# Kernel tuning notes

Hardware: AMD Instinct MI355X
Metric: run time of the kernel (lower is better)

The kernel has to match this reference:

```python
import jax, jax.numpy as jnp
import numpy as np

PATCH = 14          # ViT patch size
NUM_CLUSTERS = 64   # num_queries (cluster_strategy='fixed')
NUM_ITERS = 30      # fixed iteration budget emulating the tol-based while loop
TOL = 1e-4          # convergence tolerance on (sum of center shifts)**2
EPS = 1e-10


def _normalize(x, axis=-1, eps=EPS):
    n = jnp.linalg.norm(x, axis=axis, keepdims=True)
    return x / jnp.maximum(n, eps)


def _kmeans(X, num_clusters, key):
    """Cosine-distance k-means. X: [N, C]. Returns (assignments [N], centers [K, C])."""
    N = X.shape[0]
    idx = jax.random.choice(key, N, shape=(num_clusters,), replace=False)
    centers0 = X[idx]                       # random-point initialization
    Xn = _normalize(X)                      # normalized once, reused every iter
    ones = jnp.ones((N,), X.dtype)

    def body(carry, _):
        centers, done = carry
        # pairwise cosine distance: 1 - cos_sim  -> [N, K]
        dis = 1.0 - Xn @ _normalize(centers).T
        assign = jnp.argmin(dis, axis=1)
        # per-cluster scatter-mean (vectorized replacement of the python loop)
        sums = jax.ops.segment_sum(X, assign, num_segments=num_clusters)
        counts = jax.ops.segment_sum(ones, assign, num_segments=num_clusters)
        new_centers = jnp.where(counts[:, None] > 0,
                                sums / jnp.maximum(counts, 1.0)[:, None],
                                centers)
        shift = jnp.sum(jnp.sqrt(jnp.sum((new_centers - centers) ** 2, axis=1)))
        new_done = done | (shift ** 2 < TOL)
        centers = jnp.where(done, centers, new_centers)  # freeze after convergence
        return (centers, new_done), None

    (centers, _), _ = jax.lax.scan(body, (centers0, jnp.array(False)), None, length=NUM_ITERS)
    assign = jnp.argmin(1.0 - Xn @ _normalize(centers).T, axis=1)
    return assign, centers


def setup_inputs() -> dict:
    key = jax.random.key(0)
    features = jax.random.normal(key, (1, 1024, 96, 96), dtype=jnp.float32)
    return {"features": features}


def reference(features):
    B, C, HP, WP = features.shape  # [1, 1024, 96, 96]
    X = features.transpose(0, 2, 3, 1).reshape(-1, C)  # [N, C], N = HP*WP
    _, centers = _kmeans(X, NUM_CLUSTERS, jax.random.key(42))
    # cluster_logits = cosine similarity between every token and every center
    logits = _normalize(X) @ _normalize(centers).T            # [N, K]
    logits = logits.reshape(B, HP, WP, NUM_CLUSTERS).transpose(0, 3, 1, 2)  # [1, K, HP, WP]
    H, W = HP * PATCH, WP * PATCH
    logits_up = jax.image.resize(logits, (B, NUM_CLUSTERS, H, W), method='bilinear')
    cluster_ids = jnp.argmax(logits_up, axis=1)               # [1, H, W]
    return cluster_ids, logits_up
```

## Files before the change

kernel.cpp:

```cpp
#include <hip/hip_runtime.h>
#include <stdint.h>

#define NN 9216
#define CCH 1024
#define KK 64
#define HP 96
#define SCALE 14
#define HH 1344
#define NUM_ITERS 30
#define TOLV 1e-4

typedef __attribute__((ext_vector_type(4))) double d4;

__device__ __forceinline__ void tf2x32(unsigned k0, unsigned k1, unsigned& x0, unsigned& x1) {
  unsigned ks2 = k0 ^ k1 ^ 0x1BD11BDAu;
  x0 += k0; x1 += k1;
#define TFR(r) { x0 += x1; x1 = (x1 << r) | (x1 >> (32 - r)); x1 ^= x0; }
  TFR(13) TFR(15) TFR(26) TFR(6)
  x0 += k1; x1 += ks2 + 1u;
  TFR(17) TFR(29) TFR(16) TFR(24)
  x0 += ks2; x1 += k0 + 2u;
  TFR(13) TFR(15) TFR(26) TFR(6)
  x0 += k0; x1 += k1 + 3u;
  TFR(17) TFR(29) TFR(16) TFR(24)
  x0 += k1; x1 += ks2 + 4u;
  TFR(13) TFR(15) TFR(26) TFR(6)
  x0 += ks2; x1 += k0 + 5u;
#undef TFR
}

__global__ __launch_bounds__(256) void k_rng(unsigned* bits1, unsigned* bits2, double* ssq) {
  int t = blockIdx.x * 256 + threadIdx.x;
  unsigned k1a = 0, k1b = 0; tf2x32(0u, 42u, k1a, k1b);
  unsigned s1a = 0, s1b = 1; tf2x32(0u, 42u, s1a, s1b);
  unsigned s2a = 0, s2b = 1; tf2x32(k1a, k1b, s2a, s2b);
  unsigned o0 = 0, o1 = (unsigned)t;
  tf2x32(s1a, s1b, o0, o1);
  bits1[t] = o0 ^ o1;
  o0 = 0; o1 = (unsigned)t;
  tf2x32(s2a, s2b, o0, o1);
  bits2[t] = o0 ^ o1;
  ssq[t] = 0.0;
}

__global__ __launch_bounds__(256) void k_rank(const unsigned* __restrict__ bits,
                                              const unsigned* __restrict__ vals,
                                              unsigned* __restrict__ out_perm) {
  __shared__ __align__(16) unsigned lb[NN];
  int tid = threadIdx.x;
  for (int idx = tid; idx < NN; idx += 256) lb[idx] = bits[idx];
  __syncthreads();
  int i = blockIdx.x * 256 + tid;
  unsigned kb = lb[i];
  const uint4* l4 = reinterpret_cast<const uint4*>(lb);
  int rank = 0;
  for (int jj = 0; jj < NN / 4; ++jj) {
    uint4 v = l4[jj];
    int j = jj * 4;
    rank += (v.x < kb) || (v.x == kb && (j + 0) < i);
    rank += (v.y < kb) || (v.y == kb && (j + 1) < i);
    rank += (v.z < kb) || (v.z == kb && (j + 2) < i);
    rank += (v.w < kb) || (v.w == kb && (j + 3) < i);
  }
  out_perm[rank] = vals ? vals[i] : (unsigned)i;
}

__global__ __launch_bounds__(256) void k_gather(const float* __restrict__ F,
                                                const unsigned* __restrict__ perm2,
                                                float* __restrict__ centers) {
  int k = blockIdx.x;
  unsigned n = perm2[k];
  for (int c = threadIdx.x; c < CCH; c += 256)
    centers[k * CCH + c] = F[(size_t)c * NN + n];
}

__global__ __launch_bounds__(256) void k_ssq(const float* __restrict__ F, double* __restrict__ ssq) {
  int n = blockIdx.x * 256 + threadIdx.x;
  int c0 = blockIdx.y * 64;
  double acc = 0.0;
#pragma unroll 4
  for (int ci = 0; ci < 64; ++ci) {
    double v = (double)F[(size_t)(c0 + ci) * NN + n];
    acc = fma(v, v, acc);
  }
  atomicAdd(&ssq[n], acc);
}

__global__ __launch_bounds__(256) void k_norm32(const double* __restrict__ ssq, float* __restrict__ n32) {
  int n = blockIdx.x * 256 + threadIdx.x;
  n32[n] = (float)sqrt(ssq[n]);
}

__global__ __launch_bounds__(256) void k_prep0(const float* __restrict__ centers,
                                               float* __restrict__ cnT,
                                               int* __restrict__ counts,
                                               double* __restrict__ shift,
                                               int* __restrict__ done) {
  __shared__ double red[256];
  int k = blockIdx.x, tid = threadIdx.x;
  double local = 0.0;
  for (int c = tid; c < CCH; c += 256) {
    double v = (double)centers[k * CCH + c];
    local = fma(v, v, local);
  }
  red[tid] = local; __syncthreads();
  for (int s = 128; s > 0; s >>= 1) { if (tid < s) red[tid] += red[tid + s]; __syncthreads(); }
  float nc = fmaxf((float)sqrt(red[0]), 1e-10f);
  for (int c = tid; c < CCH; c += 256)
    cnT[(size_t)c * KK + k] = centers[k * CCH + c] / nc;
  if (tid == 0) {
    counts[k] = 0;
    if (k == 0) { *done = 0; shift[0] = 0.0; shift[1] = 0.0; }
  }
}

__global__ void k_probe(int* __restrict__ rowT, int* __restrict__ colT, int* __restrict__ okm) {
  int l = threadIdx.x;
  d4 z = {0.0, 0.0, 0.0, 0.0};
  d4 v1 = __builtin_amdgcn_mfma_f64_16x16x4f64(ldexp(1.0, l), 1.0, z, 0, 0, 0);
  d4 v2 = __builtin_amdgcn_mfma_f64_16x16x4f64(1.0, ldexp(1.0, l), z, 0, 0, 0);
  d4 v3 = __builtin_amdgcn_mfma_f64_16x16x4f64(ldexp(1.0, l >> 4), ldexp(1.0, 10 * (l >> 4)), z, 0, 0, 0);
  const double CM = 281479271743489.0;
  const double P3 = 8594130945.0;
  bool good = true, ish1 = true;
#pragma unroll
  for (int r = 0; r < 4; ++r) {
    int i = -1, j = -1;
    for (int t = 0; t < 16; ++t) {
      if (v1[r] == ldexp(CM, t)) i = t;
      if (v2[r] == ldexp(CM, t)) j = t;
    }
    good = good && (i >= 0) && (j >= 0) && (v3[r] == P3);
    ish1 = ish1 && (i == 4 * (l >> 4) + r) && (j == (l & 15));
    rowT[4 * l + r] = i; colT[4 * l + r] = j;
  }
  unsigned long long mg = __ballot(good);
  unsigned long long mh = __ballot(ish1);
  if (l == 0) *okm = (mg == ~0ull && mh != ~0ull) ? 1 : 0;
}

template <int MODE>
__global__ __launch_bounds__(256) void k_assign_m(const float* __restrict__ F,
                                                  const float* __restrict__ n32,
                                                  const float* __restrict__ cnT,
                                                  int* __restrict__ assign,
                                                  int* __restrict__ counts,
                                                  float* __restrict__ logitsS,
                                                  double* __restrict__ shift,
                                                  const int* __restrict__ done,
                                                  const int* __restrict__ rowT,
                                                  const int* __restrict__ colT,
                                                  const int* __restrict__ okm,
                                                  int iter) {
  if (*okm == 0) return;
  constexpr int CK = 64, NT = CCH / CK;
  constexpr int ASTR = 40, BSTR = 72;
  __shared__ __align__(16) float As[2][CK][ASTR];
  __shared__ __align__(16) float Bs[2][CK][BSTR];
  const int tid = threadIdx.x;
  if (MODE == 0) {
    if (blockIdx.x == 0 && tid == 0) shift[iter & 1] = 0.0;
    if (*done) return;
  }
  const int n0 = blockIdx.x * 32;
  const int s_ci = tid >> 2, s_q = tid & 3;
  const int lane = tid & 63, w = tid >> 6;
  const int h = w & 1, q = w >> 1;
  const int arow  = h * 16 + (lane & 15);
  const int kq    = lane >> 4;
  const int bcol0 = q * 32 + (lane & 15);
  float dn[8];
#pragma unroll
  for (int j = 0; j < 4; ++j) {
    dn[j]     = fmaxf(n32[n0 + 4 * s_q + j], 1e-10f);
    dn[4 + j] = fmaxf(n32[n0 + 16 + 4 * s_q + j], 1e-10f);
  }
  d4 acc0 = {0.0, 0.0, 0.0, 0.0}, acc1 = {0.0, 0.0, 0.0, 0.0};
  {
    float4 a0 = *(const float4*)(F + (size_t)s_ci * NN + n0 + 4 * s_q);
    float4 a1 = *(const float4*)(F + (size_t)s_ci * NN + n0 + 16 + 4 * s_q);
    float4 b[4];
#pragma unroll
    for (int j = 0; j < 4; ++j)
      b[j] = *(const float4*)(cnT + (size_t)s_ci * KK + 16 * s_q + 4 * j);
    float4 w0, w1;
    w0.x = a0.x / dn[0]; w0.y = a0.y / dn[1]; w0.z = a0.z / dn[2]; w0.w = a0.w / dn[3];
    w1.x = a1.x / dn[4]; w1.y = a1.y / dn[5]; w1.z = a1.z / dn[6]; w1.w = a1.w / dn[7];
    *(float4*)&As[0][s_ci][4 * s_q]      = w0;
    *(float4*)&As[0][s_ci][16 + 4 * s_q] = w1;
#pragma unroll
    for (int j = 0; j < 4; ++j)
      *(float4*)&Bs[0][s_ci][16 * s_q + 4 * j] = b[j];
  }
  __syncthreads();

  for (int t = 0; t < NT; ++t) {
    const int buf = t & 1;
    float4 a0, a1, b[4];
    if (t + 1 < NT) {
      const int cb = CK * (t + 1);
      a0 = *(const float4*)(F + (size_t)(cb + s_ci) * NN + n0 + 4 * s_q);
      a1 = *(const float4*)(F + (size_t)(cb + s_ci) * NN + n0 + 16 + 4 * s_q);
#pragma unroll
      for (int j = 0; j < 4; ++j)
        b[j] = *(const float4*)(cnT + (size_t)(cb + s_ci) * KK + 16 * s_q + 4 * j);
    }
#pragma unroll
    for (int s = 0; s < CK / 4; ++s) {
      const int ci = 4 * s + kq;
      double av = (double)As[buf][ci][arow];
      double b0 = (double)Bs[buf][ci][bcol0];
      double b1 = (double)Bs[buf][ci][bcol0 + 16];
      acc0 = __builtin_amdgcn_mfma_f64_16x16x4f64(av, b0, acc0, 0, 0, 0);
      acc1 = __builtin_amdgcn_mfma_f64_16x16x4f64(av, b1, acc1, 0, 0, 0);
    }
    if (t + 1 < NT) {
      const int nb = buf ^ 1;
      float4 w0, w1;
      w0.x = a0.x / dn[0]; w0.y = a0.y / dn[1]; w0.z = a0.z / dn[2]; w0.w = a0.w / dn[3];
      w1.x = a1.x / dn[4]; w1.y = a1.y / dn[5]; w1.z = a1.z / dn[6]; w1.w = a1.w / dn[7];
      *(float4*)&As[nb][s_ci][4 * s_q]      = w0;
      *(float4*)&As[nb][s_ci][16 + 4 * s_q] = w1;
#pragma unroll
      for (int j = 0; j < 4; ++j)
        *(float4*)&Bs[nb][s_ci][16 * s_q + 4 * j] = b[j];
    }
    __syncthreads();
  }

  float* Sl = &As[0][0][0];
#pragma unroll
  for (int r = 0; r < 4; ++r) {
    int iD = rowT[4 * lane + r];
    int jD = colT[4 * lane + r];
    Sl[(h * 16 + iD) * KK + q * 32 + jD]      = (float)acc0[r];
    Sl[(h * 16 + iD) * KK + q * 32 + 16 + jD] = (float)acc1[r];
  }
  __syncthreads();
  if (MODE == 0) {
    if (tid < 32) {
      const float* row = &Sl[tid * KK];
      float best = 1.0f - row[0]; int bk = 0;
      for (int k = 1; k < KK; ++k) { float d = 1.0f - row[k]; if (d < best) { best = d; bk = k; } }
      assign[n0 + tid] = bk;
      atomicAdd(&counts[bk], 1);
    }
  } else {
    for (int idx = tid; idx < 32 * KK; idx += 256) {
      int k = idx >> 5, nj = idx & 31;
      logitsS[(size_t)k * NN + n0 + nj] = Sl[nj * KK + k];
    }
  }
}

template <int MODE>
__global__ __launch_bounds__(256) void k_assign_v(const float* __restrict__ F,
                                                  const float* __restrict__ n32,
                                                  const float* __restrict__ cnT,
                                                  int* __restrict__ assign,
                                                  int* __restrict__ counts,
                                                  float* __restrict__ logitsS,
                                                  double* __restrict__ shift,
                                                  const int* __restrict__ done,
                                                  const int* __restrict__ okm,
                                                  int iter) {
  if (*okm != 0) return;
  constexpr int TN = 32, CK = 32, NT = CCH / CK;
  __shared__ __align__(16) float As[2][CK][TN];
  __shared__ __align__(16) float Bs[2][CK][KK];
  const int tid = threadIdx.x;
  if (MODE == 0) {
    if (blockIdx.x == 0 && tid == 0) shift[iter & 1] = 0.0;
    if (*done) return;
  }
  const int n0 = blockIdx.x * TN;
  const int a_ci = tid >> 3, a_nq = tid & 7;
  const int b_ci = tid >> 4, b_kq = tid & 15;
  const int nq = tid & 7, kp = tid >> 3;
  const float* np4 = n32 + n0 + 4 * a_nq;
  float d0 = fmaxf(np4[0], 1e-10f), d1 = fmaxf(np4[1], 1e-10f);
  float d2 = fmaxf(np4[2], 1e-10f), d3 = fmaxf(np4[3], 1e-10f);
  double acc[4][2] = {{0, 0}, {0, 0}, {0, 0}, {0, 0}};
  {
    const float* g0 = cnT + (size_t)(b_ci) * KK + 4 * b_kq;
    const float* g1 = cnT + (size_t)(16 + b_ci) * KK + 4 * b_kq;
    float* l0 = &Bs[0][0][0] + tid * 4;
    float* l1 = &Bs[0][0][0] + 1024 + tid * 4;
    __builtin_amdgcn_global_load_lds((const __attribute__((address_space(1))) void*)g0,
                                     (__attribute__((address_space(3))) void*)l0, 16, 0, 0);
    __builtin_amdgcn_global_load_lds((const __attribute__((address_space(1))) void*)g1,
                                     (__attribute__((address_space(3))) void*)l1, 16, 0, 0);
    float4 va = *(const float4*)(F + (size_t)a_ci * NN + n0 + 4 * a_nq);
    float4 w;
    w.x = va.x / d0; w.y = va.y / d1; w.z = va.z / d2; w.w = va.w / d3;
    *(float4*)(&As[0][0][0] + tid * 4) = w;
  }
  __syncthreads();

  for (int t = 0; t < NT; ++t) {
    const int buf = t & 1, nbuf = buf ^ 1;
    float4 va;
    if (t + 1 < NT) {
      const int cc = CK * (t + 1);
      const float* g0 = cnT + (size_t)(cc + b_ci) * KK + 4 * b_kq;
      const float* g1 = cnT + (size_t)(cc + 16 + b_ci) * KK + 4 * b_kq;
      float* l0 = &Bs[nbuf][0][0] + tid * 4;
      float* l1 = &Bs[nbuf][0][0] + 1024 + tid * 4;
      __builtin_amdgcn_global_load_lds((const __attribute__((address_space(1))) void*)g0,
                                       (__attribute__((address_space(3))) void*)l0, 16, 0, 0);
      __builtin_amdgcn_global_load_lds((const __attribute__((address_space(1))) void*)g1,
                                       (__attribute__((address_space(3))) void*)l1, 16, 0, 0);
      va = *(const float4*)(F + (size_t)(cc + a_ci) * NN + n0 + 4 * a_nq);
    }
#pragma unroll 8
    for (int ci = 0; ci < CK; ++ci) {
      double b0 = (double)Bs[buf][ci][2 * kp + 0], b1 = (double)Bs[buf][ci][2 * kp + 1];
      double a0 = (double)As[buf][ci][4 * nq + 0], a1 = (double)As[buf][ci][4 * nq + 1];
      double a2 = (double)As[buf][ci][4 * nq + 2], a3 = (double)As[buf][ci][4 * nq + 3];
      acc[0][0] = fma(a0, b0, acc[0][0]); acc[0][1] = fma(a0, b1, acc[0][1]);
      acc[1][0] = fma(a1, b0, acc[1][0]); acc[1][1] = fma(a1, b1, acc[1][1]);
      acc[2][0] = fma(a2, b0, acc[2][0]); acc[2][1] = fma(a2, b1, acc[2][1]);
      acc[3][0] = fma(a3, b0, acc[3][0]); acc[3][1] = fma(a3, b1, acc[3][1]);
    }
    if (t + 1 < NT) {
      float4 w;
      w.x = va.x / d0; w.y = va.y / d1; w.z = va.z / d2; w.w = va.w / d3;
      *(float4*)(&As[nbuf][0][0] + tid * 4) = w;
    }
    __syncthreads();
  }

  float* Sl = &Bs[0][0][0];
#pragma unroll
  for (int r = 0; r < 4; ++r) {
    Sl[(4 * nq + r) * KK + 2 * kp + 0] = (float)acc[r][0];
    Sl[(4 * nq + r) * KK + 2 * kp + 1] = (float)acc[r][1];
  }
  __syncthreads();
  if (MODE == 0) {
    if (tid < TN) {
      const float* row = &Sl[tid * KK];
      float best = 1.0f - row[0]; int bk = 0;
      for (int k = 1; k < KK; ++k) { float d = 1.0f - row[k]; if (d < best) { best = d; bk = k; } }
      assign[n0 + tid] = bk;
      atomicAdd(&counts[bk], 1);
    }
  } else {
    for (int idx = tid; idx < TN * KK; idx += 256) {
      int k = idx >> 5, nj = idx & 31;
      logitsS[(size_t)k * NN + n0 + nj] = Sl[nj * KK + k];
    }
  }
}

__global__ __launch_bounds__(256) void k_segsum(const float* __restrict__ F,
                                                const int* __restrict__ assign,
                                                double* __restrict__ sums,
                                                const int* __restrict__ done) {
  if (*done) return;
  constexpr int NCOPY = 8, KP = KK + 2;
  __shared__ double bins[NCOPY][KP];
  int c = blockIdx.x, tid = threadIdx.x;
  int cp = tid & (NCOPY - 1);
  for (int idx = tid; idx < NCOPY * KP; idx += 256) (&bins[0][0])[idx] = 0.0;
  __syncthreads();
  for (int n = tid; n < NN; n += 256) {
    int a = assign[n];
    double v = (double)F[(size_t)c * NN + n];
    atomicAdd(&bins[cp][a], v);
  }
  __syncthreads();
  if (tid < KK) {
    double s = 0.0;
#pragma unroll
    for (int r = 0; r < NCOPY; ++r) s += bins[r][tid];
    sums[(size_t)tid * CCH + c] = s;
  }
}

__global__ __launch_bounds__(256) void k_update(float* __restrict__ centers,
                                                const double* __restrict__ sums,
                                                int* __restrict__ counts,
                                                double* __restrict__ shift,
                                                int* __restrict__ done,
                                                float* __restrict__ cnT,
                                                int iter) {
  __shared__ double red[256];
  int k = blockIdx.x, tid = threadIdx.x;
  bool mydone = false;
  if (iter > 0) {
    double s = shift[(iter - 1) & 1];
    mydone = (*done != 0) || (s * s < TOLV);
  }
  if (mydone) { if (tid == 0) *done = 1; return; }
  int cnt = counts[k];
  double local = 0.0, l2 = 0.0;
  float nc[4];
#pragma unroll
  for (int i = 0; i < 4; ++i) {
    int c = tid + 256 * i;
    float old = centers[k * CCH + c];
    float v = (cnt > 0) ? (float)(sums[k * CCH + c] / (double)cnt) : old;
    nc[i] = v;
    double d = (double)v - (double)old;
    local = fma(d, d, local);
    double dv = (double)v;
    l2 = fma(dv, dv, l2);
    centers[k * CCH + c] = v;
  }
  red[tid] = local; __syncthreads();
  for (int s = 128; s > 0; s >>= 1) { if (tid < s) red[tid] += red[tid + s]; __syncthreads(); }
  if (tid == 0) atomicAdd(&shift[iter & 1], sqrt(red[0]));
  __syncthreads();
  red[tid] = l2; __syncthreads();
  for (int s = 128; s > 0; s >>= 1) { if (tid < s) red[tid] += red[tid + s]; __syncthreads(); }
  float nrm = fmaxf((float)sqrt(red[0]), 1e-10f);
#pragma unroll
  for (int i = 0; i < 4; ++i) {
    int c = tid + 256 * i;
    cnT[(size_t)c * KK + k] = nc[i] / nrm;
  }
  if (tid == 0) counts[k] = 0;
}

__global__ __launch_bounds__(256) void k_upsample(const float* __restrict__ logitsS,
                                                  float* __restrict__ out) {
  __shared__ float P[2][KK][HP];
  const int oy = blockIdx.x;
  const int tid = threadIdx.x;
  const float inv = 1.0f / 14.0f;
  float s_y = ((float)oy + 0.5f) * inv - 0.5f;
  float fy = floorf(s_y);
  float wy1 = s_y - fy, wy0 = 1.0f - wy1;
  int y0 = (int)fy, y1 = y0 + 1;
  if (y0 < 0)      { y0 = 0;      y1 = 0;      wy0 = 1.0f; wy1 = 0.0f; }
  if (y1 > HP - 1) { y0 = HP - 1; y1 = HP - 1; wy0 = 1.0f; wy1 = 0.0f; }
  for (int idx = tid; idx < 2 * KK * HP; idx += 256) {
    int r = idx / (KK * HP);
    int rem = idx - r * (KK * HP);
    int k = rem / HP, x = rem - k * HP;
    P[r][k][x] = logitsS[(size_t)k * NN + (r ? y1 : y0) * HP + x];
  }
  __syncthreads();
  float* outL = out + (size_t)HH * HH;
  const size_t rowoff = (size_t)oy * HH;
  for (int j = 0; j < 6; ++j) {
    int ox = tid + 256 * j;
    if (ox >= HH) break;
    float s_x = ((float)ox + 0.5f) * inv - 0.5f;
    float fx = floorf(s_x);
    float wx1 = s_x - fx, wx0 = 1.0f - wx1;
    int x0 = (int)fx, x1 = x0 + 1;
    if (x0 < 0)      { x0 = 0;      x1 = 0;      wx0 = 1.0f; wx1 = 0.0f; }
    if (x1 > HP - 1) { x0 = HP - 1; x1 = HP - 1; wx0 = 1.0f; wx1 = 0.0f; }
    float best = 0.0f; int bk = 0;
    for (int k = 0; k < KK; ++k) {
      float t0 = fmaf(wy1, P[1][k][x0], wy0 * P[0][k][x0]);
      float t1 = fmaf(wy1, P[1][k][x1], wy0 * P[0][k][x1]);
      float v  = fmaf(wx1, t1, wx0 * t0);
      outL[(size_t)k * (HH * HH) + rowoff + ox] = v;
      if (k == 0 || v > best) { best = v; bk = k; }
    }
    out[rowoff + ox] = (float)bk;
  }
}

extern "C" void kernel_launch(void* const* d_in, const int* in_sizes, int n_in,
                              void* d_out, int out_size, void* d_ws, size_t ws_size,
                              hipStream_t stream) {
  const float* F = (const float*)d_in[0];
  float* out = (float*)d_out;
  char* ws = (char*)d_ws;
  double*   ssq     = (double*)(ws + 0);
  double*   shift2  = (double*)(ws + 0);
  float*    n32     = (float*)(ws + 73728);
  float*    centers = (float*)(ws + 110592);
  float*    cnT     = (float*)(ws + 372736);
  double*   sums    = (double*)(ws + 634880);
  float*    logitsS = (float*)(ws + 1159168);
  unsigned* bits1   = (unsigned*)(ws + 3518472);
  unsigned* bits2   = (unsigned*)(ws + 3555336);
  unsigned* perm1   = (unsigned*)(ws + 3592200);
  int*      rowT    = (int*)(ws + 3592208);
  int*      colT    = (int*)(ws + 3593232);
  int*      okm     = (int*)(ws + 3594256);
  unsigned* perm2   = (unsigned*)(ws + 3629064);
  int*      assign  = (int*)(ws + 3665928);
  int*      counts  = (int*)(ws + 3702792);
  int*      done    = (int*)(ws + 3703048);

  k_rng<<<36, 256, 0, stream>>>(bits1, bits2, ssq);
  k_rank<<<36, 256, 0, stream>>>(bits1, nullptr, perm1);
  k_rank<<<36, 256, 0, stream>>>(bits2, perm1, perm2);
  k_probe<<<1, 64, 0, stream>>>(rowT, colT, okm);
  k_gather<<<64, 256, 0, stream>>>(F, perm2, centers);
  k_ssq<<<dim3(36, 16), 256, 0, stream>>>(F, ssq);
  k_norm32<<<36, 256, 0, stream>>>(ssq, n32);
  k_prep0<<<64, 256, 0, stream>>>(centers, cnT, counts, shift2, done);

  for (int it = 0; it < NUM_ITERS; ++it) {
    k_assign_m<0><<<288, 256, 0, stream>>>(F, n32, cnT, assign, counts, logitsS, shift2, done, rowT, colT, okm, it);
    k_assign_v<0><<<288, 256, 0, stream>>>(F, n32, cnT, assign, counts, logitsS, shift2, done, okm, it);
    k_segsum<<<1024, 256, 0, stream>>>(F, assign, sums, done);
    k_update<<<64, 256, 0, stream>>>(centers, sums, counts, shift2, done, cnT, it);
  }
  k_assign_m<1><<<288, 256, 0, stream>>>(F, n32, cnT, assign, counts, logitsS, shift2, done, rowT, colT, okm, 0);
  k_assign_v<1><<<288, 256, 0, stream>>>(F, n32, cnT, assign, counts, logitsS, shift2, done, okm, 0);
  k_upsample<<<1344, 256, 0, stream>>>(logitsS, out);
}
```

Measured before the change: 2.663 ms.

## Retile MFMA assign kernel to 48-token blocks and drop fallback and prep kernels

The MFMA assignment kernel now covers 48 tokens per block with each wave owning 16 centers, so each B value read from shared memory feeds three MFMAs. The grid shrinks from 288 to 192 blocks. The scalar fallback kernel is removed, the probe no longer requires a non-identity layout, the RNG is folded into the rank kernels, and the gather is merged into the center prep. Sum-of-squares now uses per-slice partial sums instead of atomics. This cuts launches and shared-memory traffic, but with fewer blocks the device may be less fully occupied, and there is no longer a fallback when the MFMA probe fails.

```diff
diff --git a/kernel.cpp b/kernel.cpp
--- a/kernel.cpp
+++ b/kernel.cpp
@@ -29,26 +29,22 @@
 #undef TFR
 }
 
-__global__ __launch_bounds__(256) void k_rng(unsigned* bits1, unsigned* bits2, double* ssq) {
-  int t = blockIdx.x * 256 + threadIdx.x;
-  unsigned k1a = 0, k1b = 0; tf2x32(0u, 42u, k1a, k1b);
-  unsigned s1a = 0, s1b = 1; tf2x32(0u, 42u, s1a, s1b);
-  unsigned s2a = 0, s2b = 1; tf2x32(k1a, k1b, s2a, s2b);
-  unsigned o0 = 0, o1 = (unsigned)t;
-  tf2x32(s1a, s1b, o0, o1);
-  bits1[t] = o0 ^ o1;
-  o0 = 0; o1 = (unsigned)t;
-  tf2x32(s2a, s2b, o0, o1);
-  bits2[t] = o0 ^ o1;
-  ssq[t] = 0.0;
-}
-
-__global__ __launch_bounds__(256) void k_rank(const unsigned* __restrict__ bits,
-                                              const unsigned* __restrict__ vals,
+template <int WHICH>
+__global__ __launch_bounds__(256) void k_rank(const unsigned* __restrict__ vals,
                                               unsigned* __restrict__ out_perm) {
   __shared__ __align__(16) unsigned lb[NN];
   int tid = threadIdx.x;
-  for (int idx = tid; idx < NN; idx += 256) lb[idx] = bits[idx];
+  unsigned sa, sb;
+  if (WHICH == 1) { sa = 0; sb = 1; tf2x32(0u, 42u, sa, sb); }
+  else {
+    unsigned k1a = 0, k1b = 0; tf2x32(0u, 42u, k1a, k1b);
+    sa = 0; sb = 1; tf2x32(k1a, k1b, sa, sb);
+  }
+  for (int idx = tid; idx < NN; idx += 256) {
+    unsigned o0 = 0, o1 = (unsigned)idx;
+    tf2x32(sa, sb, o0, o1);
+    lb[idx] = o0 ^ o1;
+  }
   __syncthreads();
   int i = blockIdx.x * 256 + tid;
   unsigned kb = lb[i];
@@ -65,16 +61,7 @@
   out_perm[rank] = vals ? vals[i] : (unsigned)i;
 }
 
-__global__ __launch_bounds__(256) void k_gather(const float* __restrict__ F,
-                                                const unsigned* __restrict__ perm2,
-                                                float* __restrict__ centers) {
-  int k = blockIdx.x;
-  unsigned n = perm2[k];
-  for (int c = threadIdx.x; c < CCH; c += 256)
-    centers[k * CCH + c] = F[(size_t)c * NN + n];
-}
-
-__global__ __launch_bounds__(256) void k_ssq(const float* __restrict__ F, double* __restrict__ ssq) {
+__global__ __launch_bounds__(256) void k_ssq(const float* __restrict__ F, double* __restrict__ ssq_p) {
   int n = blockIdx.x * 256 + threadIdx.x;
   int c0 = blockIdx.y * 64;
   double acc = 0.0;
@@ -83,31 +70,46 @@
     double v = (double)F[(size_t)(c0 + ci) * NN + n];
     acc = fma(v, v, acc);
   }
-  atomicAdd(&ssq[n], acc);
-}
-
-__global__ __launch_bounds__(256) void k_norm32(const double* __restrict__ ssq, float* __restrict__ n32) {
+  ssq_p[(size_t)blockIdx.y * NN + n] = acc;
+}
+
+__global__ __launch_bounds__(256) void k_norm16(const double* __restrict__ ssq_p, float* __restrict__ n32) {
   int n = blockIdx.x * 256 + threadIdx.x;
-  n32[n] = (float)sqrt(ssq[n]);
-}
-
-__global__ __launch_bounds__(256) void k_prep0(const float* __restrict__ centers,
+  double acc = 0.0;
+#pragma unroll
+  for (int r = 0; r < 16; ++r) acc += ssq_p[(size_t)r * NN + n];
+  n32[n] = (float)sqrt(acc);
+}
+
+__global__ __launch_bounds__(256) void k_prep0(const float* __restrict__ F,
+                                               const unsigned* __restrict__ perm2,
+                                               float* __restrict__ centers,
                                                float* __restrict__ cnT,
                                                int* __restrict__ counts,
                                                double* __restrict__ shift,
                                                int* __restrict__ done) {
   __shared__ double red[256];
   int k = blockIdx.x, tid = threadIdx.x;
+  unsigned n = perm2[k];
   double local = 0.0;
-  for (int c = tid; c < CCH; c += 256) {
-    double v = (double)centers[k * CCH + c];
-    local = fma(v, v, local);
+  float cv[4];
+#pragma unroll
+  for (int i = 0; i < 4; ++i) {
+    int c = tid + 256 * i;
+    float v = F[(size_t)c * NN + n];
+    cv[i] = v;
+    centers[k * CCH + c] = v;
+    double dv = (double)v;
+    local = fma(dv, dv, local);
   }
   red[tid] = local; __syncthreads();
   for (int s = 128; s > 0; s >>= 1) { if (tid < s) red[tid] += red[tid + s]; __syncthreads(); }
   float nc = fmaxf((float)sqrt(red[0]), 1e-10f);
-  for (int c = tid; c < CCH; c += 256)
-    cnT[(size_t)c * KK + k] = centers[k * CCH + c] / nc;
+#pragma unroll
+  for (int i = 0; i < 4; ++i) {
+    int c = tid + 256 * i;
+    cnT[(size_t)c * KK + k] = cv[i] / nc;
+  }
   if (tid == 0) {
     counts[k] = 0;
     if (k == 0) { *done = 0; shift[0] = 0.0; shift[1] = 0.0; }
@@ -122,7 +124,7 @@
   d4 v3 = __builtin_amdgcn_mfma_f64_16x16x4f64(ldexp(1.0, l >> 4), ldexp(1.0, 10 * (l >> 4)), z, 0, 0, 0);
   const double CM = 281479271743489.0;
   const double P3 = 8594130945.0;
-  bool good = true, ish1 = true;
+  bool good = true;
 #pragma unroll
   for (int r = 0; r < 4; ++r) {
     int i = -1, j = -1;
@@ -131,63 +133,63 @@
       if (v2[r] == ldexp(CM, t)) j = t;
     }
     good = good && (i >= 0) && (j >= 0) && (v3[r] == P3);
-    ish1 = ish1 && (i == 4 * (l >> 4) + r) && (j == (l & 15));
     rowT[4 * l + r] = i; colT[4 * l + r] = j;
   }
   unsigned long long mg = __ballot(good);
-  unsigned long long mh = __ballot(ish1);
-  if (l == 0) *okm = (mg == ~0ull && mh != ~0ull) ? 1 : 0;
+  if (l == 0) *okm = (mg == ~0ull) ? 1 : 0;
 }
 
 template <int MODE>
-__global__ __launch_bounds__(256) void k_assign_m(const float* __restrict__ F,
-                                                  const float* __restrict__ n32,
-                                                  const float* __restrict__ cnT,
-                                                  int* __restrict__ assign,
-                                                  int* __restrict__ counts,
-                                                  float* __restrict__ logitsS,
-                                                  double* __restrict__ shift,
-                                                  const int* __restrict__ done,
-                                                  const int* __restrict__ rowT,
-                                                  const int* __restrict__ colT,
-                                                  const int* __restrict__ okm,
-                                                  int iter) {
-  if (*okm == 0) return;
-  constexpr int CK = 64, NT = CCH / CK;
-  constexpr int ASTR = 40, BSTR = 72;
+__global__ __launch_bounds__(256) void k_assign(const float* __restrict__ F,
+                                                const float* __restrict__ n32,
+                                                const float* __restrict__ cnT,
+                                                int* __restrict__ assign,
+                                                int* __restrict__ counts,
+                                                float* __restrict__ logitsS,
+                                                double* __restrict__ shift,
+                                                const int* __restrict__ done,
+                                                const int* __restrict__ rowT,
+                                                const int* __restrict__ colT,
+                                                const int* __restrict__ okm,
+                                                int iter) {
+  constexpr int TN = 48, CK = 64, NT = CCH / CK;
+  constexpr int ASTR = 56, BSTR = 72;
   __shared__ __align__(16) float As[2][CK][ASTR];
   __shared__ __align__(16) float Bs[2][CK][BSTR];
   const int tid = threadIdx.x;
+  if (*okm == 0) return;
   if (MODE == 0) {
     if (blockIdx.x == 0 && tid == 0) shift[iter & 1] = 0.0;
     if (*done) return;
   }
-  const int n0 = blockIdx.x * 32;
+  const int n0 = blockIdx.x * TN;
   const int s_ci = tid >> 2, s_q = tid & 3;
   const int lane = tid & 63, w = tid >> 6;
-  const int h = w & 1, q = w >> 1;
-  const int arow  = h * 16 + (lane & 15);
-  const int kq    = lane >> 4;
-  const int bcol0 = q * 32 + (lane & 15);
-  float dn[8];
-#pragma unroll
-  for (int j = 0; j < 4; ++j) {
-    dn[j]     = fmaxf(n32[n0 + 4 * s_q + j], 1e-10f);
-    dn[4 + j] = fmaxf(n32[n0 + 16 + 4 * s_q + j], 1e-10f);
-  }
-  d4 acc0 = {0.0, 0.0, 0.0, 0.0}, acc1 = {0.0, 0.0, 0.0, 0.0};
+  const int col = lane & 15, kq = lane >> 4;
+  const int bcol = 16 * w + col;
+  float dn[12];
+#pragma unroll
+  for (int m = 0; m < 3; ++m)
+#pragma unroll
+    for (int j = 0; j < 4; ++j)
+      dn[4 * m + j] = fmaxf(n32[n0 + 16 * m + 4 * s_q + j], 1e-10f);
+  d4 acc[3] = {{0,0,0,0},{0,0,0,0},{0,0,0,0}};
+
   {
-    float4 a0 = *(const float4*)(F + (size_t)s_ci * NN + n0 + 4 * s_q);
-    float4 a1 = *(const float4*)(F + (size_t)s_ci * NN + n0 + 16 + 4 * s_q);
-    float4 b[4];
+    float4 a[3], b[4];
+#pragma unroll
+    for (int m = 0; m < 3; ++m)
+      a[m] = *(const float4*)(F + (size_t)s_ci * NN + n0 + 16 * m + 4 * s_q);
 #pragma unroll
     for (int j = 0; j < 4; ++j)
       b[j] = *(const float4*)(cnT + (size_t)s_ci * KK + 16 * s_q + 4 * j);
-    float4 w0, w1;
-    w0.x = a0.x / dn[0]; w0.y = a0.y / dn[1]; w0.z = a0.z / dn[2]; w0.w = a0.w / dn[3];
-    w1.x = a1.x / dn[4]; w1.y = a1.y / dn[5]; w1.z = a1.z / dn[6]; w1.w = a1.w / dn[7];
-    *(float4*)&As[0][s_ci][4 * s_q]      = w0;
-    *(float4*)&As[0][s_ci][16 + 4 * s_q] = w1;
+#pragma unroll
+    for (int m = 0; m < 3; ++m) {
+      float4 ww;
+      ww.x = a[m].x / dn[4*m+0]; ww.y = a[m].y / dn[4*m+1];
+      ww.z = a[m].z / dn[4*m+2]; ww.w = a[m].w / dn[4*m+3];
+      *(float4*)&As[0][s_ci][16 * m + 4 * s_q] = ww;
+    }
 #pragma unroll
     for (int j = 0; j < 4; ++j)
       *(float4*)&Bs[0][s_ci][16 * s_q + 4 * j] = b[j];
@@ -196,11 +198,12 @@
 
   for (int t = 0; t < NT; ++t) {
     const int buf = t & 1;
-    float4 a0, a1, b[4];
+    float4 a[3], b[4];
     if (t + 1 < NT) {
       const int cb = CK * (t + 1);
-      a0 = *(const float4*)(F + (size_t)(cb + s_ci) * NN + n0 + 4 * s_q);
-      a1 = *(const float4*)(F + (size_t)(cb + s_ci) * NN + n0 + 16 + 4 * s_q);
+#pragma unroll
+      for (int m = 0; m < 3; ++m)
+        a[m] = *(const float4*)(F + (size_t)(cb + s_ci) * NN + n0 + 16 * m + 4 * s_q);
 #pragma unroll
       for (int j = 0; j < 4; ++j)
         b[j] = *(const float4*)(cnT + (size_t)(cb + s_ci) * KK + 16 * s_q + 4 * j);
@@ -208,19 +211,23 @@
 #pragma unroll
     for (int s = 0; s < CK / 4; ++s) {
       const int ci = 4 * s + kq;
-      double av = (double)As[buf][ci][arow];
-      double b0 = (double)Bs[buf][ci][bcol0];
-      double b1 = (double)Bs[buf][ci][bcol0 + 16];
-      acc0 = __builtin_amdgcn_mfma_f64_16x16x4f64(av, b0, acc0, 0, 0, 0);
-      acc1 = __builtin_amdgcn_mfma_f64_16x16x4f64(av, b1, acc1, 0, 0, 0);
+      double bv = (double)Bs[buf][ci][bcol];
+      double a0 = (double)As[buf][ci][col];
+      double a1 = (double)As[buf][ci][16 + col];
+      double a2 = (double)As[buf][ci][32 + col];
+      acc[0] = __builtin_amdgcn_mfma_f64_16x16x4f64(a0, bv, acc[0], 0, 0, 0);
+      acc[1] = __builtin_amdgcn_mfma_f64_16x16x4f64(a1, bv, acc[1], 0, 0, 0);
+      acc[2] = __builtin_amdgcn_mfma_f64_16x16x4f64(a2, bv, acc[2], 0, 0, 0);
     }
     if (t + 1 < NT) {
       const int nb = buf ^ 1;
-      float4 w0, w1;
-      w0.x = a0.x / dn[0]; w0.y = a0.y / dn[1]; w0.z = a0.z / dn[2]; w0.w = a0.w / dn[3];
-      w1.x = a1.x / dn[4]; w1.y = a1.y / dn[5]; w1.z = a1.z / dn[6]; w1.w = a1.w / dn[7];
-      *(float4*)&As[nb][s_ci][4 * s_q]      = w0;
-      *(float4*)&As[nb][s_ci][16 + 4 * s_q] = w1;
+#pragma unroll
+      for (int m = 0; m < 3; ++m) {
+        float4 ww;
+        ww.x = a[m].x / dn[4*m+0]; ww.y = a[m].y / dn[4*m+1];
+        ww.z = a[m].z / dn[4*m+2]; ww.w = a[m].w / dn[4*m+3];
+        *(float4*)&As[nb][s_ci][16 * m + 4 * s_q] = ww;
+      }
 #pragma unroll
       for (int j = 0; j < 4; ++j)
         *(float4*)&Bs[nb][s_ci][16 * s_q + 4 * j] = b[j];
@@ -233,108 +240,9 @@
   for (int r = 0; r < 4; ++r) {
     int iD = rowT[4 * lane + r];
     int jD = colT[4 * lane + r];
-    Sl[(h * 16 + iD) * KK + q * 32 + jD]      = (float)acc0[r];
-    Sl[(h * 16 + iD) * KK + q * 32 + 16 + jD] = (float)acc1[r];
-  }
-  __syncthreads();
-  if (MODE == 0) {
-    if (tid < 32) {
-      const float* row = &Sl[tid * KK];
-      float best = 1.0f - row[0]; int bk = 0;
-      for (int k = 1; k < KK; ++k) { float d = 1.0f - row[k]; if (d < best) { best = d; bk = k; } }
-      assign[n0 + tid] = bk;
-      atomicAdd(&counts[bk], 1);
-    }
-  } else {
-    for (int idx = tid; idx < 32 * KK; idx += 256) {
-      int k = idx >> 5, nj = idx & 31;
-      logitsS[(size_t)k * NN + n0 + nj] = Sl[nj * KK + k];
-    }
-  }
-}
-
-template <int MODE>
-__global__ __launch_bounds__(256) void k_assign_v(const float* __restrict__ F,
-                                                  const float* __restrict__ n32,
-                                                  const float* __restrict__ cnT,
-                                                  int* __restrict__ assign,
-                                                  int* __restrict__ counts,
-                                                  float* __restrict__ logitsS,
-                                                  double* __restrict__ shift,
-                                                  const int* __restrict__ done,
-                                                  const int* __restrict__ okm,
-                                                  int iter) {
-  if (*okm != 0) return;
-  constexpr int TN = 32, CK = 32, NT = CCH / CK;
-  __shared__ __align__(16) float As[2][CK][TN];
-  __shared__ __align__(16) float Bs[2][CK][KK];
-  const int tid = threadIdx.x;
-  if (MODE == 0) {
-    if (blockIdx.x == 0 && tid == 0) shift[iter & 1] = 0.0;
-    if (*done) return;
-  }
-  const int n0 = blockIdx.x * TN;
-  const int a_ci = tid >> 3, a_nq = tid & 7;
-  const int b_ci = tid >> 4, b_kq = tid & 15;
-  const int nq = tid & 7, kp = tid >> 3;
-  const float* np4 = n32 + n0 + 4 * a_nq;
-  float d0 = fmaxf(np4[0], 1e-10f), d1 = fmaxf(np4[1], 1e-10f);
-  float d2 = fmaxf(np4[2], 1e-10f), d3 = fmaxf(np4[3], 1e-10f);
-  double acc[4][2] = {{0, 0}, {0, 0}, {0, 0}, {0, 0}};
-  {
-    const float* g0 = cnT + (size_t)(b_ci) * KK + 4 * b_kq;
-    const float* g1 = cnT + (size_t)(16 + b_ci) * KK + 4 * b_kq;
-    float* l0 = &Bs[0][0][0] + tid * 4;
-    float* l1 = &Bs[0][0][0] + 1024 + tid * 4;
-    __builtin_amdgcn_global_load_lds((const __attribute__((address_space(1))) void*)g0,
-                                     (__attribute__((address_space(3))) void*)l0, 16, 0, 0);
-    __builtin_amdgcn_global_load_lds((const __attribute__((address_space(1))) void*)g1,
-                                     (__attribute__((address_space(3))) void*)l1, 16, 0, 0);
-    float4 va = *(const float4*)(F + (size_t)a_ci * NN + n0 + 4 * a_nq);
-    float4 w;
-    w.x = va.x / d0; w.y = va.y / d1; w.z = va.z / d2; w.w = va.w / d3;
-    *(float4*)(&As[0][0][0] + tid * 4) = w;
-  }
-  __syncthreads();
-
-  for (int t = 0; t < NT; ++t) {
-    const int buf = t & 1, nbuf = buf ^ 1;
-    float4 va;
-    if (t + 1 < NT) {
-      const int cc = CK * (t + 1);
-      const float* g0 = cnT + (size_t)(cc + b_ci) * KK + 4 * b_kq;
-      const float* g1 = cnT + (size_t)(cc + 16 + b_ci) * KK + 4 * b_kq;
-      float* l0 = &Bs[nbuf][0][0] + tid * 4;
-      float* l1 = &Bs[nbuf][0][0] + 1024 + tid * 4;
-      __builtin_amdgcn_global_load_lds((const __attribute__((address_space(1))) void*)g0,
-                                       (__attribute__((address_space(3))) void*)l0, 16, 0, 0);
-      __builtin_amdgcn_global_load_lds((const __attribute__((address_space(1))) void*)g1,
-                                       (__attribute__((address_space(3))) void*)l1, 16, 0, 0);
-      va = *(const float4*)(F + (size_t)(cc + a_ci) * NN + n0 + 4 * a_nq);
-    }
-#pragma unroll 8
-    for (int ci = 0; ci < CK; ++ci) {
-      double b0 = (double)Bs[buf][ci][2 * kp + 0], b1 = (double)Bs[buf][ci][2 * kp + 1];
-      double a0 = (double)As[buf][ci][4 * nq + 0], a1 = (double)As[buf][ci][4 * nq + 1];
-      double a2 = (double)As[buf][ci][4 * nq + 2], a3 = (double)As[buf][ci][4 * nq + 3];
-      acc[0][0] = fma(a0, b0, acc[0][0]); acc[0][1] = fma(a0, b1, acc[0][1]);
-      acc[1][0] = fma(a1, b0, acc[1][0]); acc[1][1] = fma(a1, b1, acc[1][1]);
-      acc[2][0] = fma(a2, b0, acc[2][0]); acc[2][1] = fma(a2, b1, acc[2][1]);
-      acc[3][0] = fma(a3, b0, acc[3][0]); acc[3][1] = fma(a3, b1, acc[3][1]);
-    }
-    if (t + 1 < NT) {
-      float4 w;
-      w.x = va.x / d0; w.y = va.y / d1; w.z = va.z / d2; w.w = va.w / d3;
-      *(float4*)(&As[nbuf][0][0] + tid * 4) = w;
-    }
-    __syncthreads();
-  }
-
-  float* Sl = &Bs[0][0][0];
-#pragma unroll
-  for (int r = 0; r < 4; ++r) {
-    Sl[(4 * nq + r) * KK + 2 * kp + 0] = (float)acc[r][0];
-    Sl[(4 * nq + r) * KK + 2 * kp + 1] = (float)acc[r][1];
+#pragma unroll
+    for (int m = 0; m < 3; ++m)
+      Sl[(16 * m + iD) * KK + 16 * w + jD] = (float)acc[m][r];
   }
   __syncthreads();
   if (MODE == 0) {
@@ -347,7 +255,7 @@
     }
   } else {
     for (int idx = tid; idx < TN * KK; idx += 256) {
-      int k = idx >> 5, nj = idx & 31;
+      int k = idx / TN, nj = idx - k * TN;
       logitsS[(size_t)k * NN + n0 + nj] = Sl[nj * KK + k];
     }
   }
@@ -471,15 +379,13 @@
   const float* F = (const float*)d_in[0];
   float* out = (float*)d_out;
   char* ws = (char*)d_ws;
-  double*   ssq     = (double*)(ws + 0);
   double*   shift2  = (double*)(ws + 0);
   float*    n32     = (float*)(ws + 73728);
   float*    centers = (float*)(ws + 110592);
   float*    cnT     = (float*)(ws + 372736);
   double*   sums    = (double*)(ws + 634880);
   float*    logitsS = (float*)(ws + 1159168);
-  unsigned* bits1   = (unsigned*)(ws + 3518472);
-  unsigned* bits2   = (unsigned*)(ws + 3555336);
+  double*   ssq_p   = (double*)(ws + 1159168);
   unsigned* perm1   = (unsigned*)(ws + 3592200);
   int*      rowT    = (int*)(ws + 3592208);
   int*      colT    = (int*)(ws + 3593232);
@@ -489,22 +395,18 @@
   int*      counts  = (int*)(ws + 3702792);
   int*      done    = (int*)(ws + 3703048);
 
-  k_rng<<<36, 256, 0, stream>>>(bits1, bits2, ssq);
-  k_rank<<<36, 256, 0, stream>>>(bits1, nullptr, perm1);
-  k_rank<<<36, 256, 0, stream>>>(bits2, perm1, perm2);
+  k_rank<1><<<36, 256, 0, stream>>>(nullptr, perm1);
+  k_rank<2><<<36, 256, 0, stream>>>(perm1, perm2);
   k_probe<<<1, 64, 0, stream>>>(rowT, colT, okm);
-  k_gather<<<64, 256, 0, stream>>>(F, perm2, centers);
-  k_ssq<<<dim3(36, 16), 256, 0, stream>>>(F, ssq);
-  k_norm32<<<36, 256, 0, stream>>>(ssq, n32);
-  k_prep0<<<64, 256, 0, stream>>>(centers, cnT, counts, shift2, done);
+  k_ssq<<<dim3(36, 16), 256, 0, stream>>>(F, ssq_p);
+  k_norm16<<<36, 256, 0, stream>>>(ssq_p, n32);
+  k_prep0<<<64, 256, 0, stream>>>(F, perm2, centers, cnT, counts, shift2, done);
 
   for (int it = 0; it < NUM_ITERS; ++it) {
-    k_assign_m<0><<<288, 256, 0, stream>>>(F, n32, cnT, assign, counts, logitsS, shift2, done, rowT, colT, okm, it);
-    k_assign_v<0><<<288, 256, 0, stream>>>(F, n32, cnT, assign, counts, logitsS, shift2, done, okm, it);
+    k_assign<0><<<192, 256, 0, stream>>>(F, n32, cnT, assign, counts, logitsS, shift2, done, rowT, colT, okm, it);
     k_segsum<<<1024, 256, 0, stream>>>(F, assign, sums, done);
     k_update<<<64, 256, 0, stream>>>(centers, sums, counts, shift2, done, cnT, it);
   }
-  k_assign_m<1><<<288, 256, 0, stream>>>(F, n32, cnT, assign, counts, logitsS, shift2, done, rowT, colT, okm, 0);
-  k_assign_v<1><<<288, 256, 0, stream>>>(F, n32, cnT, assign, counts, logitsS, shift2, done, okm, 0);
+  k_assign<1><<<192, 256, 0, stream>>>(F, n32, cnT, assign, counts, logitsS, shift2, done, rowT, colT, okm, 0);
   k_upsample<<<1344, 256, 0, stream>>>(logitsS, out);
 }
```

After: 2.582 ms. 3.0% less time.
